# Kernel optimization log

Hardware: AMD Instinct MI355X
Metric: run time of the kernel (lower is better)

## Reference

```python
import jax, jax.numpy as jnp
import numpy as np

TAU = 2.0      # config.init_tau
VTH = 1.0      # config.v_threshold
VRESET = 0.0   # config.v_reset (hard reset)
ALPHA = 2.0    # ATan surrogate alpha
EPS = 1e-5     # BatchNorm eps

@jax.custom_vjp
def heaviside(x):
    return (x >= 0.0).astype(x.dtype)

def _h_fwd(x):
    return heaviside(x), x

def _h_bwd(x, g):
    # ATan surrogate gradient: alpha/2 / (1 + (pi/2*alpha*x)^2)
    return (g * (ALPHA / 2.0) / (1.0 + (jnp.pi / 2.0 * ALPHA * x) ** 2),)

heaviside.defvjp(_h_fwd, _h_bwd)

def lif_multistep(x_seq):
    """Multi-step LIF, decay_input=False, hard reset, detach_reset=True.
    x_seq: [T, ...]; returns spike train [T, ...]."""
    def step(v, x):
        v = v - (v - VRESET) / TAU + x           # leaky integrate (input not decayed)
        s = heaviside(v - VTH)                   # fire
        sd = jax.lax.stop_gradient(s)            # detach_reset
        v = (1.0 - sd) * v + sd * VRESET         # hard reset
        return v, s
    v0 = jnp.full_like(x_seq[0], VRESET)
    _, s_seq = jax.lax.scan(step, v0, x_seq)
    return s_seq

def setup_inputs() -> dict:
    key = jax.random.key(0)
    k1, k2 = jax.random.split(key)
    T, B, N = 16, 128, 2048
    x = jax.random.normal(k1, (T, B, N), dtype=jnp.float32)
    W = jax.random.normal(k2, (N, N), dtype=jnp.float32) / np.float32(np.sqrt(N))
    gamma = jnp.ones((N,), dtype=jnp.float32)
    beta = jnp.zeros((N,), dtype=jnp.float32)
    return {"x": x, "W": W, "gamma": gamma, "beta": beta}

def reference(x, W, gamma, beta):
    # x: [T, B, N]
    x_res = x
    spatial_sum = x.sum(axis=-1, keepdims=True)   # [T, B, 1]
    temporal_sum = x.sum(axis=0, keepdims=True)   # [1, B, N]
    # Linear (no bias), step_mode='m': applied per (t, b)
    h = jnp.einsum('tbn,mn->tbm', x, W)
    # BatchNorm1d over (T*B) per feature, training-mode batch stats
    mu = h.mean(axis=(0, 1))
    var = h.var(axis=(0, 1))
    h = (h - mu) * jax.lax.rsqrt(var + EPS) * gamma + beta
    # LIF2 (dropout disabled: use_dp=False)
    h = lif_multistep(h)
    sp = lif_multistep(h * spatial_sum)           # spatial_lif, broadcast to [T,B,N]
    tp = lif_multistep(h * temporal_sum)          # temporal_lif, broadcast to [T,B,N]
    return x_res + sp * tp
```

## Files before the change

### kernel.cpp

```cpp
#include <hip/hip_runtime.h>
#include <math.h>

#define T_DIM 16
#define B_DIM 128
#define N_DIM 2048
#define TB    (T_DIM * B_DIM)

#define WS_H      0
#define WS_PSUM   16777216
#define WS_PSUM2  17301504
#define WS_SSUM   17825792

typedef __attribute__((ext_vector_type(8))) short short8;
typedef __attribute__((ext_vector_type(4))) float f32x4;

#define PLANE 4194304ull
__device__ __align__(16) unsigned short g_planes[6ull * PLANE];

__device__ __forceinline__ double probeA(int m, int k) {
    return (double)((m * 7 + k * 13) % 23 - 11);
}
__device__ __forceinline__ double probeB(int k, int n) {
    return (double)((k * 5 + n * 3) % 19 - 9);
}

__device__ __forceinline__ unsigned bf16_rne(float f, float* back) {
    unsigned u = __float_as_uint(f);
    unsigned r = u + 0x7FFFu + ((u >> 16) & 1u);
    unsigned h = r >> 16;
    *back = __uint_as_float(h << 16);
    return h;
}

__device__ __forceinline__ void gload16(const unsigned short* g, char* l) {
    __builtin_amdgcn_global_load_lds(
        (const __attribute__((address_space(1))) void*)g,
        (__attribute__((address_space(3))) void*)l, 16, 0, 0);
}

__global__ __launch_bounds__(256)
void split_kernel(const float* __restrict__ x, const float* __restrict__ W,
                  double* __restrict__ ssum) {
    const int row = blockIdx.x;
    const int tid = threadIdx.x;
    const int mat = row >> 11;
    const int r   = row & 2047;
    const float* src = (mat ? W : x) + (size_t)r * N_DIM;
    unsigned short* p0 = g_planes + (size_t)(3 * mat) * PLANE
                       + (size_t)r * N_DIM + tid * 8;

    float4 f0 = *(const float4*)(src + tid * 8);
    float4 f1 = *(const float4*)(src + tid * 8 + 4);
    float v[8] = {f0.x, f0.y, f0.z, f0.w, f1.x, f1.y, f1.z, f1.w};
    unsigned h0[8], h1[8], h2[8];
    double s = 0.0;
#pragma unroll
    for (int e = 0; e < 8; ++e) {
        float b;
        h0[e] = bf16_rne(v[e], &b); float r1 = v[e] - b;
        h1[e] = bf16_rne(r1, &b);   float r2 = r1 - b;
        h2[e] = bf16_rne(r2, &b);
        s += (double)v[e];
    }
    uint4 u;
    u.x = h0[0] | (h0[1] << 16); u.y = h0[2] | (h0[3] << 16);
    u.z = h0[4] | (h0[5] << 16); u.w = h0[6] | (h0[7] << 16);
    *(uint4*)(p0) = u;
    u.x = h1[0] | (h1[1] << 16); u.y = h1[2] | (h1[3] << 16);
    u.z = h1[4] | (h1[5] << 16); u.w = h1[6] | (h1[7] << 16);
    *(uint4*)(p0 + PLANE) = u;
    u.x = h2[0] | (h2[1] << 16); u.y = h2[2] | (h2[3] << 16);
    u.z = h2[4] | (h2[5] << 16); u.w = h2[6] | (h2[7] << 16);
    *(uint4*)(p0 + 2 * PLANE) = u;

    if (mat == 0) {
        for (int off = 32; off > 0; off >>= 1) s += __shfl_down(s, off, 64);
        __shared__ double wsum[4];
        int lane = tid & 63, wv = tid >> 6;
        if (lane == 0) wsum[wv] = s;
        __syncthreads();
        if (tid == 0) ssum[r] = (wsum[0] + wsum[1]) + (wsum[2] + wsum[3]);
    }
}

__device__ unsigned probe_bf16(float* crefF, int l) {
    int i0 = l >> 2, j0 = (l & 3) << 2;
    for (int jj = 0; jj < 4; ++jj) {
        double s = 0.0;
        for (int k = 0; k < 32; ++k) s += probeA(i0, k) * probeB(k, j0 + jj);
        crefF[i0 * 16 + j0 + jj] = (float)s;
    }
    __syncthreads();
    short8 af, bf;
#pragma unroll
    for (int j = 0; j < 8; ++j) {
        int k = 8 * (l >> 4) + j;
        af[j] = (short)(__float_as_uint((float)probeA(l & 15, k)) >> 16);
        bf[j] = (short)(__float_as_uint((float)probeB(k, l & 15)) >> 16);
    }
    unsigned win = 0xFFFFFFFFu;
    for (int s = 0; s < 2; ++s) {
        f32x4 d = {0.f, 0.f, 0.f, 0.f};
        d = __builtin_amdgcn_mfma_f32_16x16x32_bf16(s ? bf : af, s ? af : bf,
                                                    d, 0, 0, 0);
        for (int dF = 0; dF < 4; ++dF) {
            float err = 0.f;
#pragma unroll
            for (int r = 0; r < 4; ++r) {
                int ii, jj;
                if (dF == 0)      { ii = 4 * (l >> 4) + r; jj = l & 15; }
                else if (dF == 1) { ii = (l >> 4) + 4 * r; jj = l & 15; }
                else if (dF == 2) { jj = 4 * (l >> 4) + r; ii = l & 15; }
                else              { jj = (l >> 4) + 4 * r; ii = l & 15; }
                err = fmaxf(err, fabsf(d[r] - crefF[ii * 16 + jj]));
            }
            for (int off = 1; off < 64; off <<= 1)
                err = fmaxf(err, __shfl_xor(err, off, 64));
            if (err < 0.5f && win == 0xFFFFFFFFu) win = (unsigned)(s * 4 + dF);
        }
    }
    return win;
}

#define MF(a, b, c) __builtin_amdgcn_mfma_f32_16x16x32_bf16((a), (b), (c), 0, 0, 0)
#define NSTEP 64
#define BUFB  24576

#define SIX_AB                                                        \
    acc[f][g] = MF(av[0][f], bv[0][g], acc[f][g]);                    \
    acc[f][g] = MF(av[0][f], bv[1][g], acc[f][g]);                    \
    acc[f][g] = MF(av[1][f], bv[0][g], acc[f][g]);                    \
    acc[f][g] = MF(av[1][f], bv[1][g], acc[f][g]);                    \
    acc[f][g] = MF(av[0][f], bv[2][g], acc[f][g]);                    \
    acc[f][g] = MF(av[2][f], bv[0][g], acc[f][g]);

#define SIX_BA                                                        \
    acc[f][g] = MF(bv[0][g], av[0][f], acc[f][g]);                    \
    acc[f][g] = MF(bv[1][g], av[0][f], acc[f][g]);                    \
    acc[f][g] = MF(bv[0][g], av[1][f], acc[f][g]);                    \
    acc[f][g] = MF(bv[1][g], av[1][f], acc[f][g]);                    \
    acc[f][g] = MF(bv[2][g], av[0][f], acc[f][g]);                    \
    acc[f][g] = MF(bv[0][g], av[2][f], acc[f][g]);

#define KLOOP(SIX)                                                    \
    for (int st = 0; st < NSTEP; ++st) {                              \
        const int cb = (st & 1) * BUFB;                               \
        if (st + 1 < NSTEP) {                                         \
            const int nb = ((st + 1) & 1) * BUFB;                     \
            _Pragma("unroll")                                         \
            for (int ii = 0; ii < 6; ++ii)                            \
                gload16(gsrc[ii] + (st + 1) * 32, smem + nb + ldso[ii]); \
        }                                                             \
        short8 av[3][2], bv[3][2];                                    \
        _Pragma("unroll")                                             \
        for (int p = 0; p < 3; ++p)                                   \
            _Pragma("unroll")                                         \
            for (int f = 0; f < 2; ++f) {                             \
                av[p][f] = *(const short8*)(smem + cb + p * 4096 + f * 1024 + aoffL); \
                bv[p][f] = *(const short8*)(smem + cb + p * 4096 + f * 1024 + boffL); \
            }                                                         \
        _Pragma("unroll")                                             \
        for (int f = 0; f < 2; ++f)                                   \
            _Pragma("unroll")                                         \
            for (int g = 0; g < 2; ++g) { SIX }                       \
        __syncthreads();                                              \
    }

__global__ __launch_bounds__(256, 2)
void gemm_bf16(const float* __restrict__ x, const float* __restrict__ W,
               float* __restrict__ C, double* __restrict__ psum,
               double* __restrict__ psum2) {
    __shared__ __align__(16) char smem[49152];
    const int t    = threadIdx.x;
    const int lane = t & 63;
    const int w    = t >> 6;
    const int wr   = w >> 1, wc = w & 1;

    const int bid = blockIdx.y * 32 + blockIdx.x;
    const int xcd = bid & 7, ii0 = bid >> 3;
    const int bx = (xcd & 3) * 8 + (ii0 & 7);
    const int by = (xcd >> 2) * 16 + (ii0 >> 3);
    const int row0 = by * 64;
    const int col0 = bx * 64;
    const int band = by;

    const unsigned win = probe_bf16((float*)smem, lane);
    __syncthreads();

    if (win <= 7u) {
        const int swp = win >> 2, dF = win & 3;
        int iD[4], jD[4];
#pragma unroll
        for (int r = 0; r < 4; ++r) {
            if (dF == 0)      { iD[r] = 4 * (lane >> 4) + r; jD[r] = lane & 15; }
            else if (dF == 1) { iD[r] = (lane >> 4) + 4 * r; jD[r] = lane & 15; }
            else if (dF == 2) { jD[r] = 4 * (lane >> 4) + r; iD[r] = lane & 15; }
            else              { jD[r] = (lane >> 4) + 4 * r; iD[r] = lane & 15; }
        }

        const unsigned short* gsrc[6];
        int ldso[6];
#pragma unroll
        for (int ii = 0; ii < 6; ++ii) {
            int i   = w + ii * 4;
            int m   = (i >= 12) ? 1 : 0;
            int r12 = i - 12 * m;
            int p   = r12 >> 2, qq = r12 & 3;
            int grow = (m ? col0 : row0) + qq * 16 + (lane >> 2);
            gsrc[ii] = g_planes + (size_t)(3 * m + p) * PLANE
                     + (size_t)grow * N_DIM + (lane & 3) * 8;
            ldso[ii] = m * 12288 + p * 4096 + qq * 1024;
        }

        const int aoffL = (32 * wr + (lane & 15)) * 64 + (lane >> 4) * 16;
        const int boffL = 12288 + (32 * wc + (lane & 15)) * 64 + (lane >> 4) * 16;

        f32x4 acc[2][2];
#pragma unroll
        for (int f = 0; f < 2; ++f)
#pragma unroll
            for (int g = 0; g < 2; ++g)
                acc[f][g] = (f32x4){0.f, 0.f, 0.f, 0.f};

#pragma unroll
        for (int ii = 0; ii < 6; ++ii)
            gload16(gsrc[ii], smem + ldso[ii]);
        __syncthreads();

        if (!swp) { KLOOP(SIX_AB) } else { KLOOP(SIX_BA) }

        double* region = (double*)(smem + w * 8192);
#pragma unroll
        for (int f = 0; f < 2; ++f)
#pragma unroll
            for (int g = 0; g < 2; ++g)
#pragma unroll
                for (int r = 0; r < 4; ++r) {
                    region[(16 * f + iD[r]) * 32 + 16 * g + jD[r]] =
                        (double)acc[f][g][r];
                    C[(size_t)(row0 + 32 * wr + 16 * f + iD[r]) * N_DIM
                      + col0 + 32 * wc + 16 * g + jD[r]] = (float)acc[f][g][r];
                }
        {
            const int c = lane & 31, half = lane >> 5;
            double s = 0.0, q = 0.0;
#pragma unroll
            for (int r = 0; r < 16; ++r) {
                double v = region[(16 * half + r) * 32 + c];
                s += v;
                q = fma(v, v, q);
            }
            s += __shfl_xor(s, 32, 64);
            q += __shfl_xor(q, 32, 64);
            double* pbuf = (double*)(smem + 32768);
            if (lane < 32) {
                pbuf[(w * 2 + 0) * 32 + c] = s;
                pbuf[(w * 2 + 1) * 32 + c] = q;
            }
        }
        __syncthreads();
        if (t < 64) {
            const int c2 = t & 31, wcc = t >> 5;
            double* pbuf = (double*)(smem + 32768);
            double s = pbuf[(wcc * 2 + 0) * 32 + c2]
                     + pbuf[((wcc + 2) * 2 + 0) * 32 + c2];
            double q = pbuf[(wcc * 2 + 1) * 32 + c2]
                     + pbuf[((wcc + 2) * 2 + 1) * 32 + c2];
            psum [band * N_DIM + col0 + 32 * wcc + c2] = s;
            psum2[band * N_DIM + col0 + 32 * wcc + c2] = q;
        }
    } else {
        for (int off = t; off < 64 * 64; off += 256) {
            int rr = off >> 6, cc = off & 63;
            const float* xr = x + (size_t)(row0 + rr) * N_DIM;
            const float* wr2 = W + (size_t)(col0 + cc) * N_DIM;
            double s = 0.0;
            for (int k = 0; k < N_DIM; ++k)
                s += (double)xr[k] * (double)wr2[k];
            C[(size_t)(row0 + rr) * N_DIM + col0 + cc] = (float)s;
        }
        __syncthreads();
        if (t < 64) {
            double s = 0.0, q = 0.0;
            for (int rr = 0; rr < 64; ++rr) {
                double v = (double)C[(size_t)(row0 + rr) * N_DIM + col0 + t];
                s += v;
                q = fma(v, v, q);
            }
            psum [band * N_DIM + col0 + t] = s;
            psum2[band * N_DIM + col0 + t] = q;
        }
    }
}

__global__ __launch_bounds__(256)
void fused_lif_kernel(const float* __restrict__ x, const float* __restrict__ h,
                      const double* __restrict__ psum, const double* __restrict__ psum2,
                      const float* __restrict__ gamma, const float* __restrict__ beta,
                      const double* __restrict__ ssum, float* __restrict__ out) {
    int idx = blockIdx.x * 256 + threadIdx.x;
    int n = idx & (N_DIM - 1);
    int b = idx >> 11;
    double s = 0.0, s2 = 0.0;
#pragma unroll
    for (int c = 0; c < 32; ++c) {
        s  += psum [c * N_DIM + n];
        s2 += psum2[c * N_DIM + n];
    }
    double mean = s * (1.0 / 2048.0);
    double var  = s2 * (1.0 / 2048.0) - mean * mean;
    double istd = 1.0 / sqrt(var + 1e-5);
    double sc = istd * (double)gamma[n];
    double sh = (double)beta[n] - mean * sc;
    float xv[T_DIM];
    double ts = 0.0;
#pragma unroll
    for (int t = 0; t < T_DIM; ++t) {
        xv[t] = x[(size_t)(t * B_DIM + b) * N_DIM + n];
        ts += (double)xv[t];
    }
    double v1 = 0.0, v2 = 0.0, v3 = 0.0;
#pragma unroll
    for (int t = 0; t < T_DIM; ++t) {
        size_t off = (size_t)(t * B_DIM + b) * N_DIM + n;
        double hv = fma((double)h[off], sc, sh);
        v1 = v1 * 0.5 + hv;
        bool s1 = (v1 >= 1.0); if (s1) v1 = 0.0;
        double in2 = s1 ? ssum[t * B_DIM + b] : 0.0;
        v2 = v2 * 0.5 + in2;
        bool s2b = (v2 >= 1.0); if (s2b) v2 = 0.0;
        double in3 = s1 ? ts : 0.0;
        v3 = v3 * 0.5 + in3;
        bool s3 = (v3 >= 1.0); if (s3) v3 = 0.0;
        out[off] = xv[t] + ((s2b && s3) ? 1.0f : 0.0f);
    }
}

extern "C" void kernel_launch(void* const* d_in, const int* in_sizes, int n_in,
                              void* d_out, int out_size, void* d_ws, size_t ws_size,
                              hipStream_t stream) {
    const float* x     = (const float*)d_in[0];
    const float* W     = (const float*)d_in[1];
    const float* gamma = (const float*)d_in[2];
    const float* beta  = (const float*)d_in[3];
    float* out = (float*)d_out;

    char* ws = (char*)d_ws;
    float*  h     = (float*)(ws + WS_H);
    double* psum  = (double*)(ws + WS_PSUM);
    double* psum2 = (double*)(ws + WS_PSUM2);
    double* ssum  = (double*)(ws + WS_SSUM);

    split_kernel<<<4096, 256, 0, stream>>>(x, W, ssum);
    gemm_bf16<<<dim3(32, 32), 256, 0, stream>>>(x, W, h, psum, psum2);
    fused_lif_kernel<<<(B_DIM * N_DIM) / 256, 256, 0, stream>>>(
        x, h, psum, psum2, gamma, beta, ssum, out);
}
```

Before: 274.9 us.

## Enlarge GEMM tile to 128x64 with 512 threads and swizzled LDS

The bf16-split GEMM block tile grows from 64x64 to 128x64, handled by 8 waves (512 threads), which halves the grid and improves reuse of the W tile. Global-to-LDS loads are split unevenly across waves, and both the store and read offsets get an XOR swizzle to reduce LDS bank conflicts. The end-of-iteration __syncthreads is replaced by a vmcnt wait plus barrier at the top of each step. The partial-sum bands drop from 32 to 16, so the LIF kernel reads fewer partials. The larger LDS footprint (72KB) and the heavier register load from 512 threads may reduce occupancy.

```diff
diff --git a/kernel.cpp b/kernel.cpp
--- a/kernel.cpp
+++ b/kernel.cpp
@@ -124,7 +124,7 @@
 
 #define MF(a, b, c) __builtin_amdgcn_mfma_f32_16x16x32_bf16((a), (b), (c), 0, 0, 0)
 #define NSTEP 64
-#define BUFB  24576
+#define BUFB  36864
 
 #define SIX_AB                                                        \
     acc[f][g] = MF(av[0][f], bv[0][g], acc[f][g]);                    \
@@ -144,33 +144,36 @@
 
 #define KLOOP(SIX)                                                    \
     for (int st = 0; st < NSTEP; ++st) {                              \
-        const int cb = (st & 1) * BUFB;                               \
+        asm volatile("s_waitcnt vmcnt(0)" ::: "memory");              \
+        __builtin_amdgcn_s_barrier();                                 \
+        __builtin_amdgcn_sched_barrier(0);                            \
         if (st + 1 < NSTEP) {                                         \
             const int nb = ((st + 1) & 1) * BUFB;                     \
             _Pragma("unroll")                                         \
             for (int ii = 0; ii < 6; ++ii)                            \
-                gload16(gsrc[ii] + (st + 1) * 32, smem + nb + ldso[ii]); \
+                if (ii < nst)                                         \
+                    gload16(gsrc[ii] + (st + 1) * 32, smem + nb + ldso[ii]); \
         }                                                             \
+        const int cb = (st & 1) * BUFB;                               \
         short8 av[3][2], bv[3][2];                                    \
         _Pragma("unroll")                                             \
         for (int p = 0; p < 3; ++p)                                   \
             _Pragma("unroll")                                         \
             for (int f = 0; f < 2; ++f) {                             \
-                av[p][f] = *(const short8*)(smem + cb + p * 4096 + f * 1024 + aoffL); \
-                bv[p][f] = *(const short8*)(smem + cb + p * 4096 + f * 1024 + boffL); \
+                av[p][f] = *(const short8*)(smem + cb + p * 8192 + f * 1024 + aoffL); \
+                bv[p][f] = *(const short8*)(smem + cb + 24576 + p * 4096 + f * 1024 + boffL); \
             }                                                         \
         _Pragma("unroll")                                             \
         for (int f = 0; f < 2; ++f)                                   \
             _Pragma("unroll")                                         \
             for (int g = 0; g < 2; ++g) { SIX }                       \
-        __syncthreads();                                              \
-    }
-
-__global__ __launch_bounds__(256, 2)
+    }
+
+__global__ __launch_bounds__(512, 2)
 void gemm_bf16(const float* __restrict__ x, const float* __restrict__ W,
                float* __restrict__ C, double* __restrict__ psum,
                double* __restrict__ psum2) {
-    __shared__ __align__(16) char smem[49152];
+    __shared__ __align__(16) char smem[73728];
     const int t    = threadIdx.x;
     const int lane = t & 63;
     const int w    = t >> 6;
@@ -179,8 +182,8 @@
     const int bid = blockIdx.y * 32 + blockIdx.x;
     const int xcd = bid & 7, ii0 = bid >> 3;
     const int bx = (xcd & 3) * 8 + (ii0 & 7);
-    const int by = (xcd >> 2) * 16 + (ii0 >> 3);
-    const int row0 = by * 64;
+    const int by = (xcd >> 2) * 8 + (ii0 >> 3);
+    const int row0 = by * 128;
     const int col0 = bx * 64;
     const int band = by;
 
@@ -198,22 +201,39 @@
             else              { jD[r] = (lane >> 4) + 4 * r; iD[r] = lane & 15; }
         }
 
+        const int sslot = ((lane & 3) ^ ((lane >> 3) & 3)) * 8;
+        int nst;
         const unsigned short* gsrc[6];
         int ldso[6];
-#pragma unroll
-        for (int ii = 0; ii < 6; ++ii) {
-            int i   = w + ii * 4;
-            int m   = (i >= 12) ? 1 : 0;
-            int r12 = i - 12 * m;
-            int p   = r12 >> 2, qq = r12 & 3;
-            int grow = (m ? col0 : row0) + qq * 16 + (lane >> 2);
-            gsrc[ii] = g_planes + (size_t)(3 * m + p) * PLANE
-                     + (size_t)grow * N_DIM + (lane & 3) * 8;
-            ldso[ii] = m * 12288 + p * 4096 + qq * 1024;
-        }
-
-        const int aoffL = (32 * wr + (lane & 15)) * 64 + (lane >> 4) * 16;
-        const int boffL = 12288 + (32 * wc + (lane & 15)) * 64 + (lane >> 4) * 16;
+        if (w < 4) {
+            nst = 6;
+#pragma unroll
+            for (int jj = 0; jj < 6; ++jj) {
+                int j = w * 6 + jj;
+                int p = j >> 3, q = j & 7;
+                int grow = row0 + q * 16 + (lane >> 2);
+                gsrc[jj] = g_planes + (size_t)p * PLANE
+                         + (size_t)grow * N_DIM + sslot;
+                ldso[jj] = p * 8192 + q * 1024;
+            }
+        } else {
+            nst = 3;
+#pragma unroll
+            for (int jj = 0; jj < 3; ++jj) {
+                int j = (w - 4) * 3 + jj;
+                int p = j >> 2, q = j & 3;
+                int grow = col0 + q * 16 + (lane >> 2);
+                gsrc[jj] = g_planes + (size_t)(3 + p) * PLANE
+                         + (size_t)grow * N_DIM + sslot;
+                ldso[jj] = 24576 + p * 4096 + q * 1024;
+            }
+#pragma unroll
+            for (int jj = 3; jj < 6; ++jj) { gsrc[jj] = gsrc[0]; ldso[jj] = ldso[0]; }
+        }
+
+        const int rslot = ((lane >> 4) ^ ((lane >> 1) & 3)) * 16;
+        const int aoffL = 2048 * wr + (lane & 15) * 64 + rslot;
+        const int boffL = 2048 * wc + (lane & 15) * 64 + rslot;
 
         f32x4 acc[2][2];
 #pragma unroll
@@ -224,10 +244,11 @@
 
 #pragma unroll
         for (int ii = 0; ii < 6; ++ii)
-            gload16(gsrc[ii], smem + ldso[ii]);
+            if (ii < nst) gload16(gsrc[ii], smem + ldso[ii]);
+
+        if (!swp) { KLOOP(SIX_AB) } else { KLOOP(SIX_BA) }
+
         __syncthreads();
-
-        if (!swp) { KLOOP(SIX_AB) } else { KLOOP(SIX_BA) }
 
         double* region = (double*)(smem + w * 8192);
 #pragma unroll
@@ -252,7 +273,7 @@
             }
             s += __shfl_xor(s, 32, 64);
             q += __shfl_xor(q, 32, 64);
-            double* pbuf = (double*)(smem + 32768);
+            double* pbuf = (double*)(smem + 65536);
             if (lane < 32) {
                 pbuf[(w * 2 + 0) * 32 + c] = s;
                 pbuf[(w * 2 + 1) * 32 + c] = q;
@@ -260,17 +281,20 @@
         }
         __syncthreads();
         if (t < 64) {
-            const int c2 = t & 31, wcc = t >> 5;
-            double* pbuf = (double*)(smem + 32768);
-            double s = pbuf[(wcc * 2 + 0) * 32 + c2]
-                     + pbuf[((wcc + 2) * 2 + 0) * 32 + c2];
-            double q = pbuf[(wcc * 2 + 1) * 32 + c2]
-                     + pbuf[((wcc + 2) * 2 + 1) * 32 + c2];
-            psum [band * N_DIM + col0 + 32 * wcc + c2] = s;
-            psum2[band * N_DIM + col0 + 32 * wcc + c2] = q;
+            const int c = t, hc = c >> 5, cc = c & 31;
+            double* pbuf = (double*)(smem + 65536);
+            double s = 0.0, q = 0.0;
+#pragma unroll
+            for (int wr4 = 0; wr4 < 4; ++wr4) {
+                int ww = wr4 * 2 + hc;
+                s += pbuf[(ww * 2 + 0) * 32 + cc];
+                q += pbuf[(ww * 2 + 1) * 32 + cc];
+            }
+            psum [band * N_DIM + col0 + c] = s;
+            psum2[band * N_DIM + col0 + c] = q;
         }
     } else {
-        for (int off = t; off < 64 * 64; off += 256) {
+        for (int off = t; off < 128 * 64; off += 512) {
             int rr = off >> 6, cc = off & 63;
             const float* xr = x + (size_t)(row0 + rr) * N_DIM;
             const float* wr2 = W + (size_t)(col0 + cc) * N_DIM;
@@ -282,7 +306,7 @@
         __syncthreads();
         if (t < 64) {
             double s = 0.0, q = 0.0;
-            for (int rr = 0; rr < 64; ++rr) {
+            for (int rr = 0; rr < 128; ++rr) {
                 double v = (double)C[(size_t)(row0 + rr) * N_DIM + col0 + t];
                 s += v;
                 q = fma(v, v, q);
@@ -303,7 +327,7 @@
     int b = idx >> 11;
     double s = 0.0, s2 = 0.0;
 #pragma unroll
-    for (int c = 0; c < 32; ++c) {
+    for (int c = 0; c < 16; ++c) {
         s  += psum [c * N_DIM + n];
         s2 += psum2[c * N_DIM + n];
     }
@@ -352,7 +376,7 @@
     double* ssum  = (double*)(ws + WS_SSUM);
 
     split_kernel<<<4096, 256, 0, stream>>>(x, W, ssum);
-    gemm_bf16<<<dim3(32, 32), 256, 0, stream>>>(x, W, h, psum, psum2);
+    gemm_bf16<<<dim3(32, 16), 512, 0, stream>>>(x, W, h, psum, psum2);
     fused_lif_kernel<<<(B_DIM * N_DIM) / 256, 256, 0, stream>>>(
         x, h, psum, psum2, gamma, beta, ssum, out);
 }
```

Result: faster. 236.0 us (-14.1%).
